# Kernel tuning notes

Hardware: AMD Instinct MI355X
Metric: run time of the kernel (lower is better)

The kernel has to match this reference:

```python
import jax, jax.numpy as jnp
import numpy as np

B, L, P, D, C, S = 32768, 256, 1024, 50, 3, 10  # batch, latent, n_protos, proto_size, classes, slots/class
EPS = 1e-5
IN_EPS = 1e-5  # torch InstanceNorm1d default eps


def _instance_norm(h):
    # torch InstanceNorm1d on (N, 50): unbatched (C, L) semantics -> normalize each row
    # over the feature axis with biased variance, no affine.
    m = jnp.mean(h, axis=-1, keepdims=True)
    v = jnp.mean((h - m) ** 2, axis=-1, keepdims=True)
    return (h - m) * jax.lax.rsqrt(v + IN_EPS)


def _project(z, W1, b1, W2, b2):
    # Linear(256->50) -> InstanceNorm1d -> ReLU -> Linear(50->50)
    h = z @ W1.T + b1
    h = jax.nn.relu(_instance_norm(h))
    return h @ W2.T + b2


def setup_inputs() -> dict:
    key = jax.random.key(0)
    ks = jax.random.split(key, 6)
    x = jax.random.normal(ks[0], (B, L), dtype=jnp.float32)
    prototypes = jax.random.normal(ks[1], (P, L), dtype=jnp.float32)
    # xavier_normal_(gain=1) on (C, P, S): std = sqrt(2 / (fan_in + fan_out)) = sqrt(2/(P+S))
    proto_presence = jax.random.normal(ks[2], (C, P, S), dtype=jnp.float32) * np.sqrt(2.0 / (P + S)).astype(np.float32)
    W1 = jax.random.normal(ks[3], (D, L), dtype=jnp.float32) * np.sqrt(1.0 / L).astype(np.float32)
    b1 = jnp.zeros((D,), jnp.float32)
    W2 = jax.random.normal(ks[4], (D, D), dtype=jnp.float32) * np.sqrt(1.0 / D).astype(np.float32)
    b2 = jnp.zeros((D,), jnp.float32)
    # class_identity_layer weight: Wc[c, i] = 1 if i // S == c else 0  -> (C, C*S)
    Wc = jnp.asarray((np.arange(C * S) // S == np.arange(C)[:, None]).astype(np.float32))
    return {"x": x, "gumbel_scalar": 0, "prototypes": prototypes,
            "proto_presence": proto_presence, "W1": W1, "b1": b1,
            "W2": W2, "b2": b2, "Wc": Wc}


def reference(x, gumbel_scalar, prototypes, proto_presence, W1, b1, W2, b2, Wc):
    # routing weights over prototypes (dim=1)
    if gumbel_scalar == 0:
        pp = jax.nn.softmax(proto_presence, axis=1)
    else:
        u = jax.random.uniform(jax.random.key(1), proto_presence.shape,
                               minval=1e-20, maxval=1.0, dtype=proto_presence.dtype)
        g = -jnp.log(-jnp.log(u))
        pp = jax.nn.softmax((proto_presence * gumbel_scalar + g) / 0.5, axis=1)

    xp = _project(x, W1, b1, W2, b2)            # [B, 50]
    lp = _project(prototypes, W1, b1, W2, b2)   # [P, 50] (batched per-prototype loop; row-wise InstanceNorm is identical)

    # L2 distance via ||a-b||^2 = ||a||^2 + ||b||^2 - 2 a.b (single GEMM instead of [B,50,P] broadcast)
    l2 = (jnp.sum(xp * xp, axis=-1)[:, None]
          + jnp.sum(lp * lp, axis=-1)[None, :]
          - 2.0 * (xp @ lp.T))                  # [B, P]
    l2 = jnp.maximum(l2, 0.0)  # clamp tiny negative fp residue; exact math is >= 0

    similarity = jnp.log((l2 + 1.0) / (l2 + EPS))          # [B, P]
    mixed = jnp.einsum('bp,cpn->bcn', similarity, pp)      # [B, C, S]
    out1 = mixed.reshape(x.shape[0], -1) @ Wc.T            # [B, C]
    out2 = jnp.concatenate([jnp.tanh(out1[:, :1]), jax.nn.relu(out1[:, 1:])], axis=1)
    return (out2, xp, similarity, pp)
```

## Files before the change

### kernel.cpp

```cpp
#include <hip/hip_runtime.h>
#include <cmath>

#define Bn 32768
#define Ln 256
#define Pn 1024
#define Dn 50
#define Cn 3
#define Sn 10

typedef short bf16x8 __attribute__((ext_vector_type(8)));
typedef float f32x4 __attribute__((ext_vector_type(4)));

__device__ inline unsigned short f2bf(float f) {
    unsigned int u = __float_as_uint(f);
    unsigned int r = (u + 0x7FFFu + ((u >> 16) & 1u)) >> 16;
    return (unsigned short)r;
}

__global__ void pp_softmax_kernel(const float* __restrict__ pres, float* __restrict__ pp,
                                  float* __restrict__ pps) {
    int c = blockIdx.x / Sn;
    int n = blockIdx.x % Sn;
    int lane = threadIdx.x;
    const float* src = pres + (size_t)c * Pn * Sn + n;
    float* dst = pp + (size_t)c * Pn * Sn + n;
    float v[16];
    float mx = -1e30f;
#pragma unroll
    for (int i = 0; i < 16; ++i) { v[i] = src[(size_t)(lane + i * 64) * Sn]; mx = fmaxf(mx, v[i]); }
#pragma unroll
    for (int m = 1; m < 64; m <<= 1) mx = fmaxf(mx, __shfl_xor(mx, m, 64));
    float sum = 0.f;
#pragma unroll
    for (int i = 0; i < 16; ++i) { v[i] = __expf(v[i] - mx); sum += v[i]; }
#pragma unroll
    for (int m = 1; m < 64; m <<= 1) sum += __shfl_xor(sum, m, 64);
    float inv = 1.0f / sum;
#pragma unroll
    for (int i = 0; i < 16; ++i) {
        float r = v[i] * inv;
        dst[(size_t)(lane + i * 64) * Sn] = r;
        atomicAdd(&pps[c * Pn + lane + i * 64], r);
    }
}

__global__ __launch_bounds__(256) void project_kernel(
    const float* __restrict__ zin,
    const float* __restrict__ W1, const float* __restrict__ b1,
    const float* __restrict__ W2, const float* __restrict__ b2,
    float* __restrict__ outp, float* __restrict__ outn,
    unsigned short* __restrict__ outb)
{
    __shared__ float xs[64][68];
    __shared__ float w1t[64][68];
    __shared__ float w2t[52][68];

    int t = threadIdx.x;
    int tx = t & 15, ty = t >> 4;
    int row0 = blockIdx.x * 64;

    for (int idx = t; idx < 52 * 64; idx += 256) {
        int j = idx & 63, k = idx >> 6;
        w2t[k][j] = (j < Dn && k < Dn) ? W2[j * Dn + k] : 0.f;
    }

    float acc[4][4] = {};
    for (int kc = 0; kc < Ln; kc += 64) {
        __syncthreads();
        for (int idx = t; idx < 64 * 64; idx += 256) {
            int kk = idx & 63, r = idx >> 6;
            xs[r][kk] = zin[(size_t)(row0 + r) * Ln + kc + kk];
        }
        for (int idx = t; idx < 64 * 64; idx += 256) {
            int j = idx & 63, kk = idx >> 6;
            w1t[kk][j] = (j < Dn) ? W1[j * Ln + kc + kk] : 0.f;
        }
        __syncthreads();
#pragma unroll 4
        for (int k4 = 0; k4 < 16; ++k4) {
            float4 xv[4], wv[4];
#pragma unroll
            for (int i = 0; i < 4; ++i) xv[i] = *(const float4*)&xs[ty * 4 + i][k4 * 4];
#pragma unroll
            for (int kk = 0; kk < 4; ++kk) wv[kk] = *(const float4*)&w1t[k4 * 4 + kk][tx * 4];
#pragma unroll
            for (int i = 0; i < 4; ++i)
#pragma unroll
                for (int kk = 0; kk < 4; ++kk)
#pragma unroll
                    for (int j = 0; j < 4; ++j)
                        acc[i][j] += (&xv[i].x)[kk] * (&wv[kk].x)[j];
        }
    }

    float rb1[4], rb2[4];
    bool valid[4];
#pragma unroll
    for (int j = 0; j < 4; ++j) {
        int c = tx * 4 + j;
        valid[j] = c < Dn;
        rb1[j] = valid[j] ? b1[c] : 0.f;
        rb2[j] = valid[j] ? b2[c] : 0.f;
    }

    __syncthreads();

#pragma unroll
    for (int i = 0; i < 4; ++i) {
        float h[4];
        float s = 0.f;
#pragma unroll
        for (int j = 0; j < 4; ++j) { h[j] = acc[i][j] + rb1[j]; s += h[j]; }
#pragma unroll
        for (int m = 1; m < 16; m <<= 1) s += __shfl_xor(s, m, 64);
        float mean = s * (1.0f / Dn);
        float s2 = 0.f;
#pragma unroll
        for (int j = 0; j < 4; ++j) { float dv = valid[j] ? (h[j] - mean) : 0.f; s2 += dv * dv; }
#pragma unroll
        for (int m = 1; m < 16; m <<= 1) s2 += __shfl_xor(s2, m, 64);
        float rstd = rsqrtf(s2 * (1.0f / Dn) + 1e-5f);
        float4 rv;
#pragma unroll
        for (int j = 0; j < 4; ++j)
            (&rv.x)[j] = valid[j] ? fmaxf((h[j] - mean) * rstd, 0.f) : 0.f;
        *(float4*)&xs[ty * 4 + i][tx * 4] = rv;
    }
    __syncthreads();

    float acc2[4][4] = {};
#pragma unroll 4
    for (int k4 = 0; k4 < 13; ++k4) {
        float4 xv[4], wv[4];
#pragma unroll
        for (int i = 0; i < 4; ++i) xv[i] = *(const float4*)&xs[ty * 4 + i][k4 * 4];
#pragma unroll
        for (int kk = 0; kk < 4; ++kk) wv[kk] = *(const float4*)&w2t[k4 * 4 + kk][tx * 4];
#pragma unroll
        for (int i = 0; i < 4; ++i)
#pragma unroll
            for (int kk = 0; kk < 4; ++kk)
#pragma unroll
                for (int j = 0; j < 4; ++j)
                    acc2[i][j] += (&xv[i].x)[kk] * (&wv[kk].x)[j];
    }

#pragma unroll
    for (int i = 0; i < 4; ++i) {
        int row = row0 + ty * 4 + i;
        float o[4];
        float q = 0.f;
#pragma unroll
        for (int j = 0; j < 4; ++j) {
            o[j] = acc2[i][j] + rb2[j];
            if (valid[j]) q += o[j] * o[j];
            if (valid[j]) outp[(size_t)row * Dn + tx * 4 + j] = o[j];
        }
        ushort4 ob;
        ob.x = valid[0] ? f2bf(o[0]) : 0;
        ob.y = valid[1] ? f2bf(o[1]) : 0;
        ob.z = valid[2] ? f2bf(o[2]) : 0;
        ob.w = valid[3] ? f2bf(o[3]) : 0;
        *(ushort4*)&outb[(size_t)row * 64 + tx * 4] = ob;
#pragma unroll
        for (int m = 1; m < 16; m <<= 1) q += __shfl_xor(q, m, 64);
        if (tx == 0) outn[row] = q;
    }
}

struct ProtoTile {
    bf16x8 b0, b1;
    float ln, p0, p1, p2;
};

__device__ __forceinline__ void load_tile(ProtoTile& T,
    const unsigned short* __restrict__ lpb, const float* __restrict__ lpn,
    const float* __restrict__ pps, int pc, int lr, int lg)
{
    T.b0 = *(const bf16x8*)&lpb[(size_t)(pc + lr) * 64 + lg * 8];
    T.b1 = *(const bf16x8*)&lpb[(size_t)(pc + lr) * 64 + 32 + lg * 8];
    T.ln = lpn[pc + lr];
    T.p0 = pps[pc + lr];
    T.p1 = pps[Pn + pc + lr];
    T.p2 = pps[2 * Pn + pc + lr];
}

__device__ __forceinline__ void compute_tile(const ProtoTile& T,
    const bf16x8 af[2][2], const float xnr[2][4], float oacc[2][4][3],
    float* __restrict__ sim, int row0, int pc, int lr, int lg)
{
    f32x4 acc[2];
#pragma unroll
    for (int m = 0; m < 2; ++m) { f32x4 z = {0.f, 0.f, 0.f, 0.f}; acc[m] = z; }
#pragma unroll
    for (int m = 0; m < 2; ++m) {
        acc[m] = __builtin_amdgcn_mfma_f32_16x16x32_bf16(af[m][0], T.b0, acc[m], 0, 0, 0);
        acc[m] = __builtin_amdgcn_mfma_f32_16x16x32_bf16(af[m][1], T.b1, acc[m], 0, 0, 0);
    }
#pragma unroll
    for (int m = 0; m < 2; ++m)
#pragma unroll
        for (int i = 0; i < 4; ++i) {
            float l2 = xnr[m][i] + T.ln - 2.f * acc[m][i];
            l2 = fmaxf(l2, 0.f);
            float s = __logf(__fdividef(l2 + 1.f, l2 + 1e-5f));
            sim[(size_t)(row0 + m * 16 + lg * 4 + i) * Pn + pc + lr] = s;
            oacc[m][i][0] += s * T.p0;
            oacc[m][i][1] += s * T.p1;
            oacc[m][i][2] += s * T.p2;
        }
}

__global__ __launch_bounds__(256) void sim_mfma_kernel(
    const unsigned short* __restrict__ xpb, const unsigned short* __restrict__ lpb,
    const float* __restrict__ xpn, const float* __restrict__ lpn,
    const float* __restrict__ pps,
    float* __restrict__ sim, float* __restrict__ out1)
{
    int t = threadIdx.x;
    int w = t >> 6, l = t & 63;
    int lr = l & 15, lg = l >> 4;
    int row0 = blockIdx.x * 32;
    int pbase = w * 256;

    bf16x8 af[2][2];
#pragma unroll
    for (int m = 0; m < 2; ++m)
#pragma unroll
        for (int ks = 0; ks < 2; ++ks)
            af[m][ks] = *(const bf16x8*)&xpb[(size_t)(row0 + m * 16 + lr) * 64 + ks * 32 + lg * 8];

    float xnr[2][4];
#pragma unroll
    for (int m = 0; m < 2; ++m)
#pragma unroll
        for (int i = 0; i < 4; ++i)
            xnr[m][i] = xpn[row0 + m * 16 + lg * 4 + i];

    float oacc[2][4][3] = {};

    ProtoTile A, B;
    load_tile(A, lpb, lpn, pps, pbase, lr, lg);

#pragma unroll
    for (int tt = 0; tt < 16; tt += 2) {
        if (tt + 1 < 16) load_tile(B, lpb, lpn, pps, pbase + (tt + 1) * 16, lr, lg);
        compute_tile(A, af, xnr, oacc, sim, row0, pbase + tt * 16, lr, lg);
        if (tt + 2 < 16) load_tile(A, lpb, lpn, pps, pbase + (tt + 2) * 16, lr, lg);
        compute_tile(B, af, xnr, oacc, sim, row0, pbase + (tt + 1) * 16, lr, lg);
    }

#pragma unroll
    for (int m = 0; m < 2; ++m)
#pragma unroll
        for (int i = 0; i < 4; ++i)
#pragma unroll
            for (int c = 0; c < 3; ++c) {
                float v = oacc[m][i][c];
                v += __shfl_xor(v, 1, 64);
                v += __shfl_xor(v, 2, 64);
                v += __shfl_xor(v, 4, 64);
                v += __shfl_xor(v, 8, 64);
                if (lr == 0)
                    atomicAdd(&out1[(size_t)(row0 + m * 16 + lg * 4 + i) * Cn + c], v);
            }
}

__global__ void finalize_kernel(const float* __restrict__ o1, float* __restrict__ out2) {
    int i = blockIdx.x * 256 + threadIdx.x;
    if (i < Bn * Cn) {
        float v = o1[i];
        int c = i - (i / Cn) * Cn;
        out2[i] = (c == 0) ? tanhf(v) : fmaxf(v, 0.f);
    }
}

extern "C" void kernel_launch(void* const* d_in, const int* in_sizes, int n_in,
                              void* d_out, int out_size, void* d_ws, size_t ws_size,
                              hipStream_t stream) {
    const float* x    = (const float*)d_in[0];
    const float* prot = (const float*)d_in[2];
    const float* pres = (const float*)d_in[3];
    const float* W1   = (const float*)d_in[4];
    const float* b1   = (const float*)d_in[5];
    const float* W2   = (const float*)d_in[6];
    const float* b2   = (const float*)d_in[7];

    float* out  = (float*)d_out;
    float* out2 = out;
    float* xp   = out + (size_t)Bn * Cn;
    float* sim  = xp + (size_t)Bn * Dn;
    float* pp   = sim + (size_t)Bn * Pn;

    float* ws     = (float*)d_ws;
    float* out1ws = ws;
    float* pps    = out1ws + (size_t)Bn * Cn;
    float* xpn    = pps + Cn * Pn;
    float* lpn    = xpn + Bn;
    float* lpf    = lpn + Pn;
    unsigned short* xpb = (unsigned short*)(lpf + Pn * Dn);
    unsigned short* lpb = xpb + (size_t)Bn * 64;

    hipMemsetAsync(out1ws, 0, ((size_t)Bn * Cn + Cn * Pn) * sizeof(float), stream);
    hipLaunchKernelGGL(pp_softmax_kernel, dim3(Cn * Sn), dim3(64), 0, stream, pres, pp, pps);
    hipLaunchKernelGGL(project_kernel, dim3(Bn / 64), dim3(256), 0, stream,
                       x, W1, b1, W2, b2, xp, xpn, xpb);
    hipLaunchKernelGGL(project_kernel, dim3(Pn / 64), dim3(256), 0, stream,
                       prot, W1, b1, W2, b2, lpf, lpn, lpb);
    hipLaunchKernelGGL(sim_mfma_kernel, dim3(Bn / 32), dim3(256), 0, stream,
                       xpb, lpb, xpn, lpn, pps, sim, out1ws);
    hipLaunchKernelGGL(finalize_kernel, dim3((Bn * Cn + 255) / 256), dim3(256), 0, stream,
                       out1ws, out2);
}
```

Measured before the change: 289.4 us.

## Pack prototype metadata into float4 and fuse finalize into sim kernel via LDS reduction

After: 287.7 us. No clear change (-0.6%).

```diff
diff --git a/kernel.cpp b/kernel.cpp
--- a/kernel.cpp
+++ b/kernel.cpp
@@ -18,7 +18,7 @@
 }
 
 __global__ void pp_softmax_kernel(const float* __restrict__ pres, float* __restrict__ pp,
-                                  float* __restrict__ pps) {
+                                  float* __restrict__ lmeta) {
     int c = blockIdx.x / Sn;
     int n = blockIdx.x % Sn;
     int lane = threadIdx.x;
@@ -39,8 +39,9 @@
 #pragma unroll
     for (int i = 0; i < 16; ++i) {
         float r = v[i] * inv;
-        dst[(size_t)(lane + i * 64) * Sn] = r;
-        atomicAdd(&pps[c * Pn + lane + i * 64], r);
+        int p = lane + i * 64;
+        dst[(size_t)p * Sn] = r;
+        atomicAdd(&lmeta[p * 4 + 1 + c], r);
     }
 }
 
@@ -48,7 +49,7 @@
     const float* __restrict__ zin,
     const float* __restrict__ W1, const float* __restrict__ b1,
     const float* __restrict__ W2, const float* __restrict__ b2,
-    float* __restrict__ outp, float* __restrict__ outn,
+    float* __restrict__ outp, float* __restrict__ outn, int nstride,
     unsigned short* __restrict__ outb)
 {
     __shared__ float xs[64][68];
@@ -164,25 +165,22 @@
         *(ushort4*)&outb[(size_t)row * 64 + tx * 4] = ob;
 #pragma unroll
         for (int m = 1; m < 16; m <<= 1) q += __shfl_xor(q, m, 64);
-        if (tx == 0) outn[row] = q;
+        if (tx == 0) outn[row * nstride] = q;
     }
 }
 
 struct ProtoTile {
     bf16x8 b0, b1;
-    float ln, p0, p1, p2;
+    float4 meta;
 };
 
 __device__ __forceinline__ void load_tile(ProtoTile& T,
-    const unsigned short* __restrict__ lpb, const float* __restrict__ lpn,
-    const float* __restrict__ pps, int pc, int lr, int lg)
+    const unsigned short* __restrict__ lpb, const float4* __restrict__ lmeta,
+    int pc, int lr, int lg)
 {
     T.b0 = *(const bf16x8*)&lpb[(size_t)(pc + lr) * 64 + lg * 8];
     T.b1 = *(const bf16x8*)&lpb[(size_t)(pc + lr) * 64 + 32 + lg * 8];
-    T.ln = lpn[pc + lr];
-    T.p0 = pps[pc + lr];
-    T.p1 = pps[Pn + pc + lr];
-    T.p2 = pps[2 * Pn + pc + lr];
+    T.meta = lmeta[pc + lr];
 }
 
 __device__ __forceinline__ void compute_tile(const ProtoTile& T,
@@ -201,28 +199,31 @@
     for (int m = 0; m < 2; ++m)
 #pragma unroll
         for (int i = 0; i < 4; ++i) {
-            float l2 = xnr[m][i] + T.ln - 2.f * acc[m][i];
+            float l2 = xnr[m][i] + T.meta.x - 2.f * acc[m][i];
             l2 = fmaxf(l2, 0.f);
             float s = __logf(__fdividef(l2 + 1.f, l2 + 1e-5f));
             sim[(size_t)(row0 + m * 16 + lg * 4 + i) * Pn + pc + lr] = s;
-            oacc[m][i][0] += s * T.p0;
-            oacc[m][i][1] += s * T.p1;
-            oacc[m][i][2] += s * T.p2;
+            oacc[m][i][0] += s * T.meta.y;
+            oacc[m][i][1] += s * T.meta.z;
+            oacc[m][i][2] += s * T.meta.w;
         }
 }
 
 __global__ __launch_bounds__(256) void sim_mfma_kernel(
     const unsigned short* __restrict__ xpb, const unsigned short* __restrict__ lpb,
-    const float* __restrict__ xpn, const float* __restrict__ lpn,
-    const float* __restrict__ pps,
-    float* __restrict__ sim, float* __restrict__ out1)
+    const float* __restrict__ xpn, const float4* __restrict__ lmeta,
+    float* __restrict__ sim, float* __restrict__ out2)
 {
+    __shared__ float redc[96];
+
     int t = threadIdx.x;
     int w = t >> 6, l = t & 63;
     int lr = l & 15, lg = l >> 4;
     int row0 = blockIdx.x * 32;
     int pbase = w * 256;
 
+    if (t < 96) redc[t] = 0.f;
+
     bf16x8 af[2][2];
 #pragma unroll
     for (int m = 0; m < 2; ++m)
@@ -232,21 +233,23 @@
 
     float xnr[2][4];
 #pragma unroll
-    for (int m = 0; m < 2; ++m)
-#pragma unroll
-        for (int i = 0; i < 4; ++i)
-            xnr[m][i] = xpn[row0 + m * 16 + lg * 4 + i];
+    for (int m = 0; m < 2; ++m) {
+        float4 xv = *(const float4*)&xpn[row0 + m * 16 + lg * 4];
+        xnr[m][0] = xv.x; xnr[m][1] = xv.y; xnr[m][2] = xv.z; xnr[m][3] = xv.w;
+    }
 
     float oacc[2][4][3] = {};
 
     ProtoTile A, B;
-    load_tile(A, lpb, lpn, pps, pbase, lr, lg);
+    load_tile(A, lpb, lmeta, pbase, lr, lg);
+
+    __syncthreads();
 
 #pragma unroll
     for (int tt = 0; tt < 16; tt += 2) {
-        if (tt + 1 < 16) load_tile(B, lpb, lpn, pps, pbase + (tt + 1) * 16, lr, lg);
+        if (tt + 1 < 16) load_tile(B, lpb, lmeta, pbase + (tt + 1) * 16, lr, lg);
         compute_tile(A, af, xnr, oacc, sim, row0, pbase + tt * 16, lr, lg);
-        if (tt + 2 < 16) load_tile(A, lpb, lpn, pps, pbase + (tt + 2) * 16, lr, lg);
+        if (tt + 2 < 16) load_tile(A, lpb, lmeta, pbase + (tt + 2) * 16, lr, lg);
         compute_tile(B, af, xnr, oacc, sim, row0, pbase + (tt + 1) * 16, lr, lg);
     }
 
@@ -262,16 +265,14 @@
                 v += __shfl_xor(v, 4, 64);
                 v += __shfl_xor(v, 8, 64);
                 if (lr == 0)
-                    atomicAdd(&out1[(size_t)(row0 + m * 16 + lg * 4 + i) * Cn + c], v);
+                    atomicAdd(&redc[(m * 16 + lg * 4 + i) * 3 + c], v);
             }
-}
-
-__global__ void finalize_kernel(const float* __restrict__ o1, float* __restrict__ out2) {
-    int i = blockIdx.x * 256 + threadIdx.x;
-    if (i < Bn * Cn) {
-        float v = o1[i];
-        int c = i - (i / Cn) * Cn;
-        out2[i] = (c == 0) ? tanhf(v) : fmaxf(v, 0.f);
+
+    __syncthreads();
+    if (t < 96) {
+        int c = t - (t / 3) * 3;
+        float v = redc[t];
+        out2[(size_t)row0 * 3 + t] = (c == 0) ? tanhf(v) : fmaxf(v, 0.f);
     }
 }
 
@@ -293,22 +294,18 @@
     float* pp   = sim + (size_t)Bn * Pn;
 
     float* ws     = (float*)d_ws;
-    float* out1ws = ws;
-    float* pps    = out1ws + (size_t)Bn * Cn;
-    float* xpn    = pps + Cn * Pn;
-    float* lpn    = xpn + Bn;
-    float* lpf    = lpn + Pn;
+    float* lmeta  = ws;
+    float* xpn    = lmeta + (size_t)Pn * 4;
+    float* lpf    = xpn + Bn;
     unsigned short* xpb = (unsigned short*)(lpf + Pn * Dn);
     unsigned short* lpb = xpb + (size_t)Bn * 64;
 
-    hipMemsetAsync(out1ws, 0, ((size_t)Bn * Cn + Cn * Pn) * sizeof(float), stream);
-    hipLaunchKernelGGL(pp_softmax_kernel, dim3(Cn * Sn), dim3(64), 0, stream, pres, pp, pps);
+    hipMemsetAsync(lmeta, 0, (size_t)Pn * 4 * sizeof(float), stream);
+    hipLaunchKernelGGL(pp_softmax_kernel, dim3(Cn * Sn), dim3(64), 0, stream, pres, pp, lmeta);
     hipLaunchKernelGGL(project_kernel, dim3(Bn / 64), dim3(256), 0, stream,
-                       x, W1, b1, W2, b2, xp, xpn, xpb);
+                       x, W1, b1, W2, b2, xp, xpn, 1, xpb);
     hipLaunchKernelGGL(project_kernel, dim3(Pn / 64), dim3(256), 0, stream,
-                       prot, W1, b1, W2, b2, lpf, lpn, lpb);
+                       prot, W1, b1, W2, b2, lpf, lmeta, 4, lpb);
     hipLaunchKernelGGL(sim_mfma_kernel, dim3(Bn / 32), dim3(256), 0, stream,
-                       xpb, lpb, xpn, lpn, pps, sim, out1ws);
-    hipLaunchKernelGGL(finalize_kernel, dim3((Bn * Cn + 255) / 256), dim3(256), 0, stream,
-                       out1ws, out2);
-}
+                       xpb, lpb, xpn, (const float4*)lmeta, sim, out2);
+}
```
